# Performance work log

Hardware: AMD Instinct MI355X
Metric: run time of the kernel (lower is better)

The kernel has to match this reference:

```python
import jax, jax.numpy as jnp
import numpy as np

VOC, EDIM, HDIM, SSZ, SDIM, SDEPTH, PAD = 32000, 256, 256, 128, 128, 2, 0
N, BSZ = 64, 32
T = 2 * N - 1  # 127
N_ACTS = 2  # push, pop


def _linear(key, out_d, in_d):
    k1, k2 = jax.random.split(key)
    return (jax.random.normal(k1, (out_d, in_d), jnp.float32) * 0.02,
            jax.random.normal(k2, (out_d,), jnp.float32) * 0.02)


def setup_inputs() -> dict:
    key = jax.random.key(0)
    ks = jax.random.split(key, 9)
    emb_W = jax.random.normal(ks[0], (VOC, EDIM), jnp.float32) * 0.02
    emb_W = emb_W.at[PAD].set(0.0)  # padding_idx row is zero in torch
    W_e2h, b_e2h = _linear(ks[1], HDIM, EDIM)
    W_s2h, b_s2h = _linear(ks[2], HDIM, SDIM * SDEPTH)
    W_h2h, b_h2h = _linear(ks[3], HDIM, HDIM)
    W_h2i, b_h2i = _linear(ks[4], N_ACTS + 1, HDIM)
    W_h2s, b_h2s = _linear(ks[5], SDIM, HDIM)
    W_s2u, b_s2u = _linear(ks[6], SDIM, SDIM * SDEPTH)
    empty_elem = jax.random.normal(ks[7], (1, SDIM), jnp.float32) * 0.02
    inputs = jax.random.randint(ks[8], (N, BSZ), 0, VOC)
    return dict(inputs=inputs, emb_W=emb_W, W_e2h=W_e2h, b_e2h=b_e2h,
                W_s2h=W_s2h, b_s2h=b_s2h, W_h2h=W_h2h, b_h2h=b_h2h,
                W_h2i=W_h2i, b_h2i=b_h2i, W_h2s=W_h2s, b_h2s=b_h2s,
                W_s2u=W_s2u, b_s2u=b_s2u, empty_elem=empty_elem)


def _srnn(inputs, emb_W, W_e2h, b_e2h, W_s2h, b_s2h, W_h2h, b_h2h,
          W_h2i, b_h2i, W_h2s, b_h2s, W_s2u, b_s2u, empty_elem):
    bsz = inputs.shape[1]
    embs = emb_W[inputs]                                        # [N, bsz, edim]
    pads = jnp.broadcast_to(emb_W[PAD], (T - N, bsz, EDIM))     # padded tail
    buf0 = jnp.concatenate([embs, pads], axis=0)                # [T, bsz, edim]
    hid0 = jnp.zeros((bsz, HDIM), jnp.float32)
    stack0 = jnp.broadcast_to(empty_elem, (bsz, SSZ, SDIM))

    def step(carry, t):
        hid, stack, buf = carry
        tops = stack[:, :SDEPTH, :].reshape(bsz, SDEPTH * SDIM)
        inp = buf[t]                                            # [bsz, edim]
        ihid = inp @ W_e2h.T + b_e2h + tops @ W_s2h.T + b_s2h
        hid = jax.nn.relu(hid @ W_h2h.T + b_h2h + ihid)
        inst = ihid @ W_h2i.T + b_h2i                           # [bsz, 3]
        act = jax.nn.softmax(inst[:, :N_ACTS], axis=-1)
        gamma = 1.0 + jnp.log1p(jnp.exp(inst[:, N_ACTS:]))      # [bsz, 1]
        a = act ** gamma
        a = a / (jnp.sum(a, axis=-1, keepdims=True) + 1e-16)    # sharpened acts
        p_push, p_pop = a[:, :1], a[:, 1:]                      # [bsz, 1]
        # buffer update: pop shifts the whole buffer down one slot along time
        buf_pop = jnp.concatenate([jnp.zeros_like(buf[:1]), buf[:-1]], axis=0)
        buf = p_push[None] * buf + p_pop[None] * buf_pop        # [1,bsz,1] bcast
        push_val = jax.nn.relu(hid @ W_h2s.T + b_h2s)           # [bsz, sdim]
        u_val = jax.nn.relu(tops @ W_s2u.T + b_s2u)             # [bsz, sdim]
        z = jnp.zeros((bsz, 1, SDIM), jnp.float32)
        # W_push (shift down by 1) as an index roll
        stack_push = jnp.concatenate([z, stack[:, :-1, :]], axis=1)
        stack_push = stack_push.at[:, 0, :].add(push_val)
        # W_pop = shift up by SDEPTH, then W_push = shift down by 1
        up = jnp.concatenate([stack[:, SDEPTH:, :],
                              jnp.zeros((bsz, SDEPTH, SDIM), jnp.float32)], axis=1)
        stack_pop = jnp.concatenate([z, up[:, :-1, :]], axis=1)
        stack_pop = stack_pop.at[:, 0, :].add(u_val)
        stack_pop = stack_pop.at[:, SSZ - SDEPTH + 1:, :].add(empty_elem[0])
        stack = p_push[:, :, None] * stack_push + p_pop[:, :, None] * stack_pop
        return (hid, stack, buf), (hid, a, stack[:, 0, :])

    (hid, stack, _), (outputs, acts, top_elems) = jax.lax.scan(
        step, (hid0, stack0, buf0), jnp.arange(T))
    return outputs, hid, stack, acts, top_elems


def reference(inputs, emb_W, W_e2h, b_e2h, W_s2h, b_s2h, W_h2h, b_h2h,
              W_h2i, b_h2i, W_h2s, b_h2s, W_s2u, b_s2u, empty_elem):
    return _srnn(inputs, emb_W, W_e2h, b_e2h, W_s2h, b_s2h, W_h2h, b_h2h,
                 W_h2i, b_h2i, W_h2s, b_h2s, W_s2u, b_s2u, empty_elem)
```

## Files before the change

kernel.cpp:

```cpp
#include <hip/hip_runtime.h>
#include <stdint.h>
#include <math.h>


#define T_STEPS 127

#define OUT_OFF   0
#define HID_OFF   1040384
#define STACK_OFF 1048576
#define ACTS_OFF  1572864
#define TE_OFF    1580992

#define W3_OFF 16384
#define W2_OFF 20480
#define E2H_OFF_U 131072

typedef _Float16 h2 __attribute__((ext_vector_type(2)));

__device__ __forceinline__ unsigned packh2(float a, float b){
  h2 v; v.x = (_Float16)a; v.y = (_Float16)b;
  return __builtin_bit_cast(unsigned, v);
}
__device__ __forceinline__ float h2loF(unsigned u){ h2 v = __builtin_bit_cast(h2,u); return (float)v.x; }
__device__ __forceinline__ float h2hiF(unsigned u){ h2 v = __builtin_bit_cast(h2,u); return (float)v.y; }

#if __has_builtin(__builtin_amdgcn_fdot2)
__device__ __forceinline__ float fdot2(unsigned a, unsigned b, float c){
  return __builtin_amdgcn_fdot2(__builtin_bit_cast(h2,a), __builtin_bit_cast(h2,b), c, false);
}
#else
__device__ __forceinline__ float fdot2(unsigned a, unsigned b, float c){
  return c + h2loF(a)*h2loF(b) + h2hiF(a)*h2hiF(b);
}
#endif

#define CHOFF(u) (12*((u)>>3) + ((u)&7))
#define STGP(p)  (20*((p)>>3) + 2*((p)&7))

__global__ void prep_all(const int* __restrict__ inputs, const float* __restrict__ embW,
                         const float* __restrict__ We2h,
                         const float* __restrict__ Ws2h, const float* __restrict__ Wh2h,
                         const float* __restrict__ Wh2s, const float* __restrict__ Ws2u,
                         uint4* __restrict__ out4, unsigned* __restrict__ e2hpk){
  int tid = threadIdx.x;
  int bi  = blockIdx.x;
  if (bi >= 256){
    int gid = (bi-256)*256 + tid;
    const float* src;
    if (gid < 16384){
      int i = gid >> 10, t_ = gid & 1023;
      const float* S = (t_ < 512) ? Ws2h : Wh2h;
      int r = t_ & 511, jp = r >> 2, ks = r & 3;
      int j  = 2*jp + (i >> 3);
      int k0 = ks*64 + (i & 7)*8;
      src = S + j*256 + k0;
    } else {
      int l = gid - 16384;
      int region = l >> 12, li = l & 4095;
      int i = li >> 9, rB = li & 511;
      int jp = rB >> 3, ks = rB & 7;
      int j  = 2*jp + (i >> 2);
      int k0 = ks*32 + (i & 3)*8;
      src = (region ? Ws2u : Wh2s) + j*256 + k0;
    }
    uint4 r4;
    r4.x = packh2(src[0], src[1]); r4.y = packh2(src[2], src[3]);
    r4.z = packh2(src[4], src[5]); r4.w = packh2(src[6], src[7]);
    out4[gid] = r4;
    return;
  }
  __shared__ float emb[8][256];
  int r2 = bi >> 3, bg = bi & 7;
  for (int q=0;q<8;q++){
    int rr = q >> 2, bb = q & 3;
    int tok = inputs[(2*r2+rr)*32 + bg*4+bb];
    emb[q][tid] = embW[tok*256 + tid];
  }
  __syncthreads();
  float acc[8] = {0.f,0.f,0.f,0.f,0.f,0.f,0.f,0.f};
  for (int i8=0;i8<32;i8++){
    float4 f0 = *(const float4*)&We2h[tid*256 + i8*8];
    float4 f1 = *(const float4*)&We2h[tid*256 + i8*8 + 4];
    float wv[8] = {f0.x,f0.y,f0.z,f0.w,f1.x,f1.y,f1.z,f1.w};
    #pragma unroll
    for (int c=0;c<4;c++){
      float lo = wv[2*c], hi = wv[2*c+1];
      int k = i8*8 + c*2;
      #pragma unroll
      for (int q=0;q<8;q++)
        acc[q] += emb[q][k]*lo + emb[q][k+1]*hi;
    }
  }
  int base = (bg*4)*8192 + r2*256 + tid;
  #pragma unroll
  for (int bb=0;bb<4;bb++)
    e2hpk[base + bb*8192] = packh2(acc[bb], acc[4+bb]);
}

__global__ __attribute__((amdgpu_flat_work_group_size(1024,1024), amdgpu_waves_per_eu(4,4)))
void srnn_main(const uint4* __restrict__ ws4, const unsigned* __restrict__ wsu,
               const float* __restrict__ b_e2h, const float* __restrict__ b_s2h,
               const float* __restrict__ b_h2h, const float* __restrict__ Wh2i,
               const float* __restrict__ b_h2i, const float* __restrict__ b_h2s,
               const float* __restrict__ b_s2u, const float* __restrict__ empty_el,
               float* __restrict__ out)
{
  __shared__ __align__(16) float    stk_s[128*128];
  __shared__ __align__(16) unsigned e2h4[16*520];
  __shared__ __align__(16) float    halo_top[2][16*128];
  __shared__ __align__(16) float    halo_bot[2][16*128];
  __shared__ __align__(16) float    accih_st[320], acchp_st[320];
  __shared__ __align__(16) unsigned s_pk[192], hid_pk[192];
  __shared__ __align__(16) float    pv_s[128], uv_s[128];
  __shared__ __align__(16) float    whi_s[768];
  __shared__ float    wbuf[2][192];
  __shared__ unsigned pkwc[32];
  __shared__ float    pp_s, pq_s;

  const int tid = threadIdx.x;
  const int b   = blockIdx.x;
  const int aside = tid >> 9;
  const int ar  = tid & 511;
  const int ajp = ar >> 2;
  const int aks = ar & 3;
  const int rB  = tid & 511;
  const int jpB = rB >> 3;
  const int ksB = rB & 7;
  const int h2sSide = (tid >= 512);
  const int g   = tid >> 6;
  const int cp  = tid & 63;

  uint4 w1r[16], wBr[8];
  #pragma unroll
  for (int i=0;i<16;i++) w1r[i] = ws4[i*1024 + tid];
  {
    int wbase = h2sSide ? W3_OFF : W2_OFF;
    #pragma unroll
    for (int i=0;i<8;i++) wBr[i] = ws4[wbase + i*512 + rB];
  }

  float bA0=0.f, bA1=0.f;
  if (aks==0){
    int j0 = 2*ajp;
    if (aside==0){ bA0 = b_e2h[j0]+b_s2h[j0]; bA1 = b_e2h[j0+1]+b_s2h[j0+1]; }
    else         { bA0 = b_h2h[j0];           bA1 = b_h2h[j0+1]; }
  }
  float bB0=0.f, bB1=0.f;
  if (ksB==0){
    const float* bb = h2sSide ? b_h2s : b_s2u;
    bB0 = bb[2*jpB]; bB1 = bb[2*jpB+1];
  }
  const float bi0=b_h2i[0], bi1=b_h2i[1], bi2=b_h2i[2];

  const unsigned* e2hg = wsu + E2H_OFF_U + b*8192;
  #pragma unroll
  for (int q=0;q<8;q++){
    int idx = q*1024 + tid;
    int r2 = idx >> 8, j = idx & 255;
    e2h4[(r2>>1)*520 + 2*j + (r2&1)] = e2hg[idx];
  }
  const float2 emt2 = *(const float2*)&empty_el[2*cp];
  #pragma unroll
  for (int j=0;j<8;j++)
    *(float2*)&stk_s[(8*g+j)*128 + 2*cp] = emt2;
  *(float2*)&halo_top[0][g*128 + 2*cp] = emt2;
  *(float2*)&halo_bot[0][g*128 + 2*cp] = emt2;
  if (tid < 768) whi_s[tid] = Wh2i[tid];
  if (tid < 128){
    hid_pk[CHOFF(tid)] = 0u;
    int cu = tid & 63;
    s_pk[CHOFF(tid)] = packh2(empty_el[2*cu], empty_el[2*cu+1]);
  }
  if (tid < 192){ wbuf[0][tid] = (tid==64)?1.f:0.f; wbuf[1][tid]=0.f; }
  if (tid < 32)  pkwc[tid] = (tid==0)? packh2(1.f,0.f) : 0u;
  __syncthreads();

  int cur = 0;
  for (int t=0;t<T_STEPS;++t){
    {
      const unsigned* act  = aside ? hid_pk : s_pk;
      const unsigned* actB = act + 48*aks;
      float x0 = 0.f, x1 = 0.f;
      if (aside==0){
        #pragma unroll
        for (int qq=0;qq<4;qq++){
          int r2g = 4*aks + qq;
          unsigned cwE = pkwc[8*aks + 2*qq];
          unsigned cwO = pkwc[8*aks + 2*qq + 1];
          uint4 u = *(const uint4*)&e2h4[r2g*520 + 4*ajp];
          x0 = fdot2(cwE, u.x, x0); x0 = fdot2(cwO, u.y, x0);
          x1 = fdot2(cwE, u.z, x1); x1 = fdot2(cwO, u.w, x1);
        }
      }
      #pragma unroll
      for (int i=0;i<8;i++){
        uint4 A  = *(const uint4*)(actB + 12*(i>>1) + 4*(i&1));
        uint4 Wa = w1r[i], Wb = w1r[8+i];
        x0 = fdot2(A.x,Wa.x,x0); x0 = fdot2(A.y,Wa.y,x0);
        x0 = fdot2(A.z,Wa.z,x0); x0 = fdot2(A.w,Wa.w,x0);
        x1 = fdot2(A.x,Wb.x,x1); x1 = fdot2(A.y,Wb.y,x1);
        x1 = fdot2(A.z,Wb.z,x1); x1 = fdot2(A.w,Wb.w,x1);
      }
      x0 += __shfl_xor(x0,1); x0 += __shfl_xor(x0,2);
      x1 += __shfl_xor(x1,1); x1 += __shfl_xor(x1,2);
      if (aks==0){
        float* dst = aside ? acchp_st : accih_st;
        *(float2*)&dst[STGP(ajp)] = make_float2(x0 + bA0, x1 + bA1);
      }
    }
    __syncthreads();

    if (tid >= 64 && tid < 192){
      int hl = tid - 64;
      int w_ = STGP(hl);
      float2 ih2 = *(const float2*)&accih_st[w_];
      float2 hp2 = *(const float2*)&acchp_st[w_];
      float hn0 = fmaxf(ih2.x+hp2.x, 0.f);
      float hn1 = fmaxf(ih2.y+hp2.y, 0.f);
      hid_pk[CHOFF(hl)] = packh2(hn0,hn1);
      *(float2*)&out[OUT_OFF + t*8192 + b*256 + 2*hl] = make_float2(hn0,hn1);
      if (t==T_STEPS-1) *(float2*)&out[HID_OFF + b*256 + 2*hl] = make_float2(hn0,hn1);
    }

    {
      float y0=0.f, y1=0.f;
      #pragma unroll
      for (int i=0;i<4;i++){
        unsigned u0,u1,u2,u3;
        if (h2sSide){
          const int off = 40*ksB + ((i>=2)?20:0) + 8*(i&1);
          float4 a0 = *(const float4*)(accih_st + off);
          float4 a1 = *(const float4*)(accih_st + off + 4);
          float4 c0 = *(const float4*)(acchp_st + off);
          float4 c1 = *(const float4*)(acchp_st + off + 4);
          u0 = packh2(fmaxf(a0.x+c0.x,0.f), fmaxf(a0.y+c0.y,0.f));
          u1 = packh2(fmaxf(a0.z+c0.z,0.f), fmaxf(a0.w+c0.w,0.f));
          u2 = packh2(fmaxf(a1.x+c1.x,0.f), fmaxf(a1.y+c1.y,0.f));
          u3 = packh2(fmaxf(a1.z+c1.z,0.f), fmaxf(a1.w+c1.w,0.f));
        } else {
          uint4 S = *(const uint4*)&s_pk[12*(2*ksB + (i>>1)) + 4*(i&1)];
          u0 = S.x; u1 = S.y; u2 = S.z; u3 = S.w;
        }
        uint4 Wa = wBr[i], Wb = wBr[4+i];
        y0=fdot2(u0,Wa.x,y0); y0=fdot2(u1,Wa.y,y0); y0=fdot2(u2,Wa.z,y0); y0=fdot2(u3,Wa.w,y0);
        y1=fdot2(u0,Wb.x,y1); y1=fdot2(u1,Wb.y,y1); y1=fdot2(u2,Wb.z,y1); y1=fdot2(u3,Wb.w,y1);
      }
      y0 += __shfl_xor(y0,1); y0 += __shfl_xor(y0,2); y0 += __shfl_xor(y0,4);
      y1 += __shfl_xor(y1,1); y1 += __shfl_xor(y1,2); y1 += __shfl_xor(y1,4);
      if (ksB==0){
        float* dst = h2sSide ? pv_s : uv_s;
        dst[2*jpB]   = fmaxf(y0+bB0,0.f);
        dst[2*jpB+1] = fmaxf(y1+bB1,0.f);
      }
    }

    if (tid < 64){
      int l = tid;
      float4 av = *(const float4*)&accih_st[20*(l>>2) + 4*(l&3)];
      float4 q0 = *(const float4*)&whi_s[4*l];
      float4 q1 = *(const float4*)&whi_s[256 + 4*l];
      float4 q2 = *(const float4*)&whi_s[512 + 4*l];
      float p0 = av.x*q0.x + av.y*q0.y + av.z*q0.z + av.w*q0.w;
      float p1 = av.x*q1.x + av.y*q1.y + av.z*q1.z + av.w*q1.w;
      float p2 = av.x*q2.x + av.y*q2.y + av.z*q2.z + av.w*q2.w;
      #pragma unroll
      for (int o=1;o<=32;o<<=1){
        p0 += __shfl_xor(p0,o); p1 += __shfl_xor(p1,o); p2 += __shfl_xor(p2,o);
      }
      float i0 = bi0+p0, i1 = bi1+p1, gi = bi2+p2;
      float mx = fmaxf(i0,i1);
      float e0 = expf(i0-mx), e1 = expf(i1-mx);
      float inv = 1.f/(e0+e1);
      float act0 = e0*inv, act1 = e1*inv;
      float gamma = 1.f + log1pf(expf(gi));
      float A0 = powf(act0,gamma), A1 = powf(act1,gamma);
      float sden = A0+A1+1e-16f;
      if (l==0){
        float ppv = A0/sden, pqv = A1/sden;
        pp_s = ppv; pq_s = pqv;
        *(float2*)&out[ACTS_OFF + t*64 + b*2] = make_float2(ppv,pqv);
      }
    }
    __syncthreads();
    const float pp = pp_s, pq = pq_s;

    {
      float2 w[10];
      #pragma unroll
      for (int k=1;k<=8;k++)
        w[k] = *(const float2*)&stk_s[(8*g + k - 1)*128 + 2*cp];
      w[0] = (g>0)  ? *(const float2*)&halo_bot[cur][(g-1)*128 + 2*cp]
                    : make_float2(0.f,0.f);
      w[9] = (g<15) ? *(const float2*)&halo_top[cur][(g+1)*128 + 2*cp]
                    : emt2;
      float2 pv2 = make_float2(0.f,0.f), uv2 = make_float2(0.f,0.f);
      if (g == 0){ pv2 = *(const float2*)&pv_s[2*cp]; uv2 = *(const float2*)&uv_s[2*cp]; }
      float2 nn0, nn1;
      #pragma unroll
      for (int j=0;j<8;j++){
        float2 nv;
        nv.x = pp*w[j].x + pq*w[j+2].x;
        nv.y = pp*w[j].y + pq*w[j+2].y;
        if (j==0 && g==0){
          nv.x = pp*pv2.x + pq*uv2.x;
          nv.y = pp*pv2.y + pq*uv2.y;
        }
        *(float2*)&stk_s[(8*g+j)*128 + 2*cp] = nv;
        if (j==0){ nn0 = nv; *(float2*)&halo_top[cur^1][g*128 + 2*cp] = nv; }
        if (j==1){ nn1 = nv; }
        if (j==7){ *(float2*)&halo_bot[cur^1][g*128 + 2*cp] = nv; }
      }
      if (g == 0){
        *(float2*)&out[TE_OFF + t*4096 + b*128 + 2*cp] = nn0;
        s_pk[CHOFF(cp)]    = packh2(nn0.x, nn0.y);
        s_pk[CHOFF(64+cp)] = packh2(nn1.x, nn1.y);
      }
      if (tid < 128){
        int k = 64+tid;
        wbuf[cur^1][k] = pp*wbuf[cur][k] + pq*wbuf[cur][k-1];
      } else if (tid < 160){
        int r2 = tid-128;
        int k1 = 65 + t - 2*r2;
        float wa = wbuf[cur][k1], wb2 = wbuf[cur][k1-1], wc2 = wbuf[cur][k1-2];
        pkwc[r2] = packh2(pp*wa+pq*wb2, pp*wb2+pq*wc2);
      }
    }
    __syncthreads();
    cur ^= 1;
  }

  #pragma unroll
  for (int j=0;j<8;j++)
    *(float2*)&out[STACK_OFF + b*16384 + (8*g+j)*128 + 2*cp] =
      *(const float2*)&stk_s[(8*g+j)*128 + 2*cp];
}

extern "C" void kernel_launch(void* const* d_in, const int* in_sizes, int n_in,
                              void* d_out, int out_size, void* d_ws, size_t ws_size,
                              hipStream_t stream){
  const int*   inputs = (const int*)d_in[0];
  const float* embW   = (const float*)d_in[1];
  const float* We2h   = (const float*)d_in[2];
  const float* b_e2h  = (const float*)d_in[3];
  const float* Ws2h   = (const float*)d_in[4];
  const float* b_s2h  = (const float*)d_in[5];
  const float* Wh2h   = (const float*)d_in[6];
  const float* b_h2h  = (const float*)d_in[7];
  const float* Wh2i   = (const float*)d_in[8];
  const float* b_h2i  = (const float*)d_in[9];
  const float* Wh2s   = (const float*)d_in[10];
  const float* b_h2s  = (const float*)d_in[11];
  const float* Ws2u   = (const float*)d_in[12];
  const float* b_s2u  = (const float*)d_in[13];
  const float* empty  = (const float*)d_in[14];
  unsigned* wsu = (unsigned*)d_ws;

  prep_all<<<dim3(352), dim3(256), 0, stream>>>(inputs, embW, We2h, Ws2h, Wh2h,
                                                Wh2s, Ws2u, (uint4*)wsu,
                                                wsu + E2H_OFF_U);
  srnn_main<<<dim3(32), dim3(1024), 0, stream>>>((const uint4*)wsu, (const unsigned*)wsu,
                                                 b_e2h, b_s2h, b_h2h, Wh2i, b_h2i,
                                                 b_h2s, b_s2u, empty, (float*)d_out);
}
```

Baseline: 891.4 us.

## Precompute h2i projections to compute gates in parallel with matvec, cut a barrier

Folds W_h2i through W_s2h and the e2h projection on the host-side prep kernel so the push/pop gate can be computed from the stack top and token contributions directly, concurrently with the main matvec instead of after it. This removes one block-wide barrier per timestep and lets the h2s/s2u results feed the stack top row directly via a double-buffered row0 buffer. It adds a precompute block and extra workspace, and rearranges thread roles, with some risk of reduced precision from reassociation.

```diff
diff --git a/kernel.cpp b/kernel.cpp
--- a/kernel.cpp
+++ b/kernel.cpp
@@ -14,6 +14,9 @@
 #define W3_OFF 16384
 #define W2_OFF 20480
 #define E2H_OFF_U 131072
+#define E2I_F 393216
+#define P2_F  401408
+#define CVEC_F 402176
 
 typedef _Float16 h2 __attribute__((ext_vector_type(2)));
 
@@ -33,6 +36,8 @@
   return c + h2loF(a)*h2loF(b) + h2hiF(a)*h2hiF(b);
 }
 #endif
+
+#define BAR() asm volatile("s_waitcnt lgkmcnt(0)\n\ts_barrier" ::: "memory")
 
 #define CHOFF(u) (12*((u)>>3) + ((u)&7))
 #define STGP(p)  (20*((p)>>3) + 2*((p)&7))
@@ -41,10 +46,16 @@
                          const float* __restrict__ We2h,
                          const float* __restrict__ Ws2h, const float* __restrict__ Wh2h,
                          const float* __restrict__ Wh2s, const float* __restrict__ Ws2u,
-                         uint4* __restrict__ out4, unsigned* __restrict__ e2hpk){
+                         const float* __restrict__ Wh2i,
+                         const float* __restrict__ b_e2h, const float* __restrict__ b_s2h,
+                         const float* __restrict__ b_h2i,
+                         unsigned* __restrict__ wsu){
   int tid = threadIdx.x;
   int bi  = blockIdx.x;
-  if (bi >= 256){
+  uint4* out4 = (uint4*)wsu;
+  unsigned* e2hpk = wsu + E2H_OFF_U;
+  float* wsf = (float*)wsu;
+  if (bi >= 256 && bi < 352){
     int gid = (bi-256)*256 + tid;
     const float* src;
     if (gid < 16384){
@@ -69,7 +80,25 @@
     out4[gid] = r4;
     return;
   }
+  if (bi == 352){
+    int k = tid;
+    float s0=0.f, s1=0.f, s2=0.f;
+    for (int m=0;m<256;m++){
+      float wmk = Ws2h[m*256+k];
+      s0 += Wh2i[m]*wmk; s1 += Wh2i[256+m]*wmk; s2 += Wh2i[512+m]*wmk;
+    }
+    wsf[P2_F +       k] = s0;
+    wsf[P2_F + 256 + k] = s1;
+    wsf[P2_F + 512 + k] = s2;
+    if (tid < 3){
+      float c = b_h2i[tid];
+      for (int m=0;m<256;m++) c += (b_e2h[m]+b_s2h[m])*Wh2i[tid*256+m];
+      wsf[CVEC_F + tid] = c;
+    }
+    return;
+  }
   __shared__ float emb[8][256];
+  __shared__ float red[3][4][8];
   int r2 = bi >> 3, bg = bi & 7;
   for (int q=0;q<8;q++){
     int rr = q >> 2, bb = q & 3;
@@ -95,24 +124,48 @@
   #pragma unroll
   for (int bb=0;bb<4;bb++)
     e2hpk[base + bb*8192] = packh2(acc[bb], acc[4+bb]);
+  int wv_ = tid>>6, ln = tid&63;
+  for (int jj=0;jj<3;jj++){
+    float w = Wh2i[jj*256 + tid];
+    float v[8];
+    #pragma unroll
+    for (int q=0;q<8;q++) v[q] = acc[q]*w;
+    #pragma unroll
+    for (int o=1;o<=32;o<<=1){
+      #pragma unroll
+      for (int q=0;q<8;q++) v[q] += __shfl_xor(v[q],o);
+    }
+    if (ln==0){
+      #pragma unroll
+      for (int q=0;q<8;q++) red[jj][wv_][q] = v[q];
+    }
+  }
+  __syncthreads();
+  if (tid < 24){
+    int jj = tid>>3, q = tid&7;
+    float s = red[jj][0][q]+red[jj][1][q]+red[jj][2][q]+red[jj][3][q];
+    int rr = q>>2, bb = q&3;
+    wsf[E2I_F + (4*bg+bb)*256 + jj*64 + (2*r2+rr)] = s;
+  }
 }
 
 __global__ __attribute__((amdgpu_flat_work_group_size(1024,1024), amdgpu_waves_per_eu(4,4)))
 void srnn_main(const uint4* __restrict__ ws4, const unsigned* __restrict__ wsu,
                const float* __restrict__ b_e2h, const float* __restrict__ b_s2h,
-               const float* __restrict__ b_h2h, const float* __restrict__ Wh2i,
-               const float* __restrict__ b_h2i, const float* __restrict__ b_h2s,
-               const float* __restrict__ b_s2u, const float* __restrict__ empty_el,
-               float* __restrict__ out)
+               const float* __restrict__ b_h2h,
+               const float* __restrict__ b_h2s, const float* __restrict__ b_s2u,
+               const float* __restrict__ empty_el, float* __restrict__ out)
 {
   __shared__ __align__(16) float    stk_s[128*128];
   __shared__ __align__(16) unsigned e2h4[16*520];
   __shared__ __align__(16) float    halo_top[2][16*128];
   __shared__ __align__(16) float    halo_bot[2][16*128];
+  __shared__ __align__(16) float    row0_lds[2][128];
   __shared__ __align__(16) float    accih_st[320], acchp_st[320];
-  __shared__ __align__(16) unsigned s_pk[192], hid_pk[192];
-  __shared__ __align__(16) float    pv_s[128], uv_s[128];
-  __shared__ __align__(16) float    whi_s[768];
+  __shared__ __align__(16) unsigned s_pk[2][192];
+  __shared__ __align__(16) unsigned hid_pk[192];
+  __shared__ __align__(16) float    e2i_s[192];
+  __shared__ __align__(16) float    p2_s[768];
   __shared__ float    wbuf[2][192];
   __shared__ unsigned pkwc[32];
   __shared__ float    pp_s, pq_s;
@@ -123,10 +176,9 @@
   const int ar  = tid & 511;
   const int ajp = ar >> 2;
   const int aks = ar & 3;
-  const int rB  = tid & 511;
-  const int jpB = rB >> 3;
-  const int ksB = rB & 7;
-  const int h2sSide = (tid >= 512);
+  const int jpB = tid >> 4;
+  const int which = (tid >> 3) & 1;
+  const int ksB = tid & 7;
   const int g   = tid >> 6;
   const int cp  = tid & 63;
 
@@ -134,9 +186,10 @@
   #pragma unroll
   for (int i=0;i<16;i++) w1r[i] = ws4[i*1024 + tid];
   {
-    int wbase = h2sSide ? W3_OFF : W2_OFF;
+    int wbase = which ? W3_OFF : W2_OFF;
+    int rIdx  = jpB*8 + ksB;
     #pragma unroll
-    for (int i=0;i<8;i++) wBr[i] = ws4[wbase + i*512 + rB];
+    for (int i=0;i<8;i++) wBr[i] = ws4[wbase + i*512 + rIdx];
   }
 
   float bA0=0.f, bA1=0.f;
@@ -145,12 +198,11 @@
     if (aside==0){ bA0 = b_e2h[j0]+b_s2h[j0]; bA1 = b_e2h[j0+1]+b_s2h[j0+1]; }
     else         { bA0 = b_h2h[j0];           bA1 = b_h2h[j0+1]; }
   }
-  float bB0=0.f, bB1=0.f;
-  if (ksB==0){
-    const float* bb = h2sSide ? b_h2s : b_s2u;
-    bB0 = bb[2*jpB]; bB1 = bb[2*jpB+1];
-  }
-  const float bi0=b_h2i[0], bi1=b_h2i[1], bi2=b_h2i[2];
+  const float* bbB = which ? b_h2s : b_s2u;
+  const float bB0 = bbB[2*jpB], bB1 = bbB[2*jpB+1];
+  const float* wsf = (const float*)wsu;
+  float c0r=0.f, c1r=0.f, c2r=0.f;
+  if (tid >= 960){ c0r = wsf[CVEC_F]; c1r = wsf[CVEC_F+1]; c2r = wsf[CVEC_F+2]; }
 
   const unsigned* e2hg = wsu + E2H_OFF_U + b*8192;
   #pragma unroll
@@ -165,11 +217,13 @@
     *(float2*)&stk_s[(8*g+j)*128 + 2*cp] = emt2;
   *(float2*)&halo_top[0][g*128 + 2*cp] = emt2;
   *(float2*)&halo_bot[0][g*128 + 2*cp] = emt2;
-  if (tid < 768) whi_s[tid] = Wh2i[tid];
+  if (tid < 128) row0_lds[0][tid] = empty_el[tid];
+  if (tid < 192) e2i_s[tid] = wsf[E2I_F + b*256 + tid];
+  if (tid < 768) p2_s[tid] = wsf[P2_F + tid];
   if (tid < 128){
     hid_pk[CHOFF(tid)] = 0u;
     int cu = tid & 63;
-    s_pk[CHOFF(tid)] = packh2(empty_el[2*cu], empty_el[2*cu+1]);
+    s_pk[0][CHOFF(tid)] = packh2(empty_el[2*cu], empty_el[2*cu+1]);
   }
   if (tid < 192){ wbuf[0][tid] = (tid==64)?1.f:0.f; wbuf[1][tid]=0.f; }
   if (tid < 32)  pkwc[tid] = (tid==0)? packh2(1.f,0.f) : 0u;
@@ -178,7 +232,7 @@
   int cur = 0;
   for (int t=0;t<T_STEPS;++t){
     {
-      const unsigned* act  = aside ? hid_pk : s_pk;
+      const unsigned* act  = aside ? hid_pk : s_pk[cur];
       const unsigned* actB = act + 48*aks;
       float x0 = 0.f, x1 = 0.f;
       if (aside==0){
@@ -208,7 +262,55 @@
         *(float2*)&dst[STGP(ajp)] = make_float2(x0 + bA0, x1 + bA1);
       }
     }
-    __syncthreads();
+    if (tid >= 960){
+      int l = tid - 960;
+      float p0, p1, p2v;
+      if (l < 32){
+        unsigned cw = pkwc[l];
+        float cf0 = h2loF(cw), cf1 = h2hiF(cw);
+        float2 a0 = *(const float2*)&e2i_s[      2*l];
+        float2 a1 = *(const float2*)&e2i_s[ 64 + 2*l];
+        float2 a2 = *(const float2*)&e2i_s[128 + 2*l];
+        p0  = cf0*a0.x + cf1*a0.y;
+        p1  = cf0*a1.x + cf1*a1.y;
+        p2v = cf0*a2.x + cf1*a2.y;
+      } else {
+        int c = l - 32;
+        p0 = p1 = p2v = 0.f;
+        #pragma unroll
+        for (int m=0;m<4;m++){
+          int k2 = c + 32*m;
+          unsigned tp = s_pk[cur][CHOFF(k2)];
+          float t0 = h2loF(tp), t1 = h2hiF(tp);
+          float2 q0 = *(const float2*)&p2_s[      2*k2];
+          float2 q1 = *(const float2*)&p2_s[256 + 2*k2];
+          float2 q2 = *(const float2*)&p2_s[512 + 2*k2];
+          p0  += t0*q0.x + t1*q0.y;
+          p1  += t0*q1.x + t1*q1.y;
+          p2v += t0*q2.x + t1*q2.y;
+        }
+      }
+      #pragma unroll
+      for (int o=1;o<=32;o<<=1){
+        p0 += __shfl_xor(p0,o); p1 += __shfl_xor(p1,o); p2v += __shfl_xor(p2v,o);
+      }
+      if (l == 0){
+        float i0 = c0r+p0, i1 = c1r+p1, gi = c2r+p2v;
+        float mx = fmaxf(i0,i1);
+        float e0 = expf(i0-mx), e1 = expf(i1-mx);
+        float inv = 1.f/(e0+e1);
+        float act0 = e0*inv, act1 = e1*inv;
+        float gamma = 1.f + log1pf(expf(gi));
+        float A0 = powf(act0,gamma), A1 = powf(act1,gamma);
+        float sden = A0+A1+1e-16f;
+        float ppv = A0/sden, pqv = A1/sden;
+        pp_s = ppv; pq_s = pqv;
+        *(float2*)&out[ACTS_OFF + t*64 + b*2] = make_float2(ppv,pqv);
+      }
+    }
+    BAR();
+
+    const float pp = pp_s, pq = pq_s;
 
     if (tid >= 64 && tid < 192){
       int hl = tid - 64;
@@ -227,7 +329,7 @@
       #pragma unroll
       for (int i=0;i<4;i++){
         unsigned u0,u1,u2,u3;
-        if (h2sSide){
+        if (which){
           const int off = 40*ksB + ((i>=2)?20:0) + 8*(i&1);
           float4 a0 = *(const float4*)(accih_st + off);
           float4 a1 = *(const float4*)(accih_st + off + 4);
@@ -238,7 +340,7 @@
           u2 = packh2(fmaxf(a1.x+c1.x,0.f), fmaxf(a1.y+c1.y,0.f));
           u3 = packh2(fmaxf(a1.z+c1.z,0.f), fmaxf(a1.w+c1.w,0.f));
         } else {
-          uint4 S = *(const uint4*)&s_pk[12*(2*ksB + (i>>1)) + 4*(i&1)];
+          uint4 S = *(const uint4*)&s_pk[cur][12*(2*ksB + (i>>1)) + 4*(i&1)];
           u0 = S.x; u1 = S.y; u2 = S.z; u3 = S.w;
         }
         uint4 Wa = wBr[i], Wb = wBr[4+i];
@@ -247,92 +349,61 @@
       }
       y0 += __shfl_xor(y0,1); y0 += __shfl_xor(y0,2); y0 += __shfl_xor(y0,4);
       y1 += __shfl_xor(y1,1); y1 += __shfl_xor(y1,2); y1 += __shfl_xor(y1,4);
-      if (ksB==0){
-        float* dst = h2sSide ? pv_s : uv_s;
-        dst[2*jpB]   = fmaxf(y0+bB0,0.f);
-        dst[2*jpB+1] = fmaxf(y1+bB1,0.f);
-      }
-    }
-
-    if (tid < 64){
-      int l = tid;
-      float4 av = *(const float4*)&accih_st[20*(l>>2) + 4*(l&3)];
-      float4 q0 = *(const float4*)&whi_s[4*l];
-      float4 q1 = *(const float4*)&whi_s[256 + 4*l];
-      float4 q2 = *(const float4*)&whi_s[512 + 4*l];
-      float p0 = av.x*q0.x + av.y*q0.y + av.z*q0.z + av.w*q0.w;
-      float p1 = av.x*q1.x + av.y*q1.y + av.z*q1.z + av.w*q1.w;
-      float p2 = av.x*q2.x + av.y*q2.y + av.z*q2.z + av.w*q2.w;
-      #pragma unroll
-      for (int o=1;o<=32;o<<=1){
-        p0 += __shfl_xor(p0,o); p1 += __shfl_xor(p1,o); p2 += __shfl_xor(p2,o);
-      }
-      float i0 = bi0+p0, i1 = bi1+p1, gi = bi2+p2;
-      float mx = fmaxf(i0,i1);
-      float e0 = expf(i0-mx), e1 = expf(i1-mx);
-      float inv = 1.f/(e0+e1);
-      float act0 = e0*inv, act1 = e1*inv;
-      float gamma = 1.f + log1pf(expf(gi));
-      float A0 = powf(act0,gamma), A1 = powf(act1,gamma);
-      float sden = A0+A1+1e-16f;
-      if (l==0){
-        float ppv = A0/sden, pqv = A1/sden;
-        pp_s = ppv; pq_s = pqv;
-        *(float2*)&out[ACTS_OFF + t*64 + b*2] = make_float2(ppv,pqv);
-      }
-    }
-    __syncthreads();
-    const float pp = pp_s, pq = pq_s;
+      float v0 = fmaxf(y0+bB0, 0.f), v1 = fmaxf(y1+bB1, 0.f);
+      float o0 = __shfl_xor(v0, 8),  o1 = __shfl_xor(v1, 8);
+      if (!which && ksB==0){
+        float n0 = pp*o0 + pq*v0;
+        float n1 = pp*o1 + pq*v1;
+        *(float2*)&row0_lds[cur^1][2*jpB] = make_float2(n0,n1);
+        s_pk[cur^1][CHOFF(jpB)] = packh2(n0,n1);
+        *(float2*)&out[TE_OFF + t*4096 + b*128 + 2*jpB] = make_float2(n0,n1);
+      }
+    }
+
+    if (tid < 128){
+      int k = 64+tid;
+      wbuf[cur^1][k] = pp*wbuf[cur][k] + pq*wbuf[cur][k-1];
+    } else if (tid < 160){
+      int r2 = tid-128;
+      int k1 = 65 + t - 2*r2;
+      float wa = wbuf[cur][k1], wb2 = wbuf[cur][k1-1], wc2 = wbuf[cur][k1-2];
+      pkwc[r2] = packh2(pp*wa+pq*wb2, pp*wb2+pq*wc2);
+    }
 
     {
       float2 w[10];
       #pragma unroll
       for (int k=1;k<=8;k++)
         w[k] = *(const float2*)&stk_s[(8*g + k - 1)*128 + 2*cp];
+      if (g==0) w[1] = *(const float2*)&row0_lds[cur][2*cp];
       w[0] = (g>0)  ? *(const float2*)&halo_bot[cur][(g-1)*128 + 2*cp]
                     : make_float2(0.f,0.f);
       w[9] = (g<15) ? *(const float2*)&halo_top[cur][(g+1)*128 + 2*cp]
                     : emt2;
-      float2 pv2 = make_float2(0.f,0.f), uv2 = make_float2(0.f,0.f);
-      if (g == 0){ pv2 = *(const float2*)&pv_s[2*cp]; uv2 = *(const float2*)&uv_s[2*cp]; }
-      float2 nn0, nn1;
       #pragma unroll
       for (int j=0;j<8;j++){
+        if (j==0 && g==0) continue;
         float2 nv;
         nv.x = pp*w[j].x + pq*w[j+2].x;
         nv.y = pp*w[j].y + pq*w[j+2].y;
-        if (j==0 && g==0){
-          nv.x = pp*pv2.x + pq*uv2.x;
-          nv.y = pp*pv2.y + pq*uv2.y;
-        }
         *(float2*)&stk_s[(8*g+j)*128 + 2*cp] = nv;
-        if (j==0){ nn0 = nv; *(float2*)&halo_top[cur^1][g*128 + 2*cp] = nv; }
-        if (j==1){ nn1 = nv; }
-        if (j==7){ *(float2*)&halo_bot[cur^1][g*128 + 2*cp] = nv; }
-      }
-      if (g == 0){
-        *(float2*)&out[TE_OFF + t*4096 + b*128 + 2*cp] = nn0;
-        s_pk[CHOFF(cp)]    = packh2(nn0.x, nn0.y);
-        s_pk[CHOFF(64+cp)] = packh2(nn1.x, nn1.y);
-      }
-      if (tid < 128){
-        int k = 64+tid;
-        wbuf[cur^1][k] = pp*wbuf[cur][k] + pq*wbuf[cur][k-1];
-      } else if (tid < 160){
-        int r2 = tid-128;
-        int k1 = 65 + t - 2*r2;
-        float wa = wbuf[cur][k1], wb2 = wbuf[cur][k1-1], wc2 = wbuf[cur][k1-2];
-        pkwc[r2] = packh2(pp*wa+pq*wb2, pp*wb2+pq*wc2);
-      }
-    }
-    __syncthreads();
+        if (j==0) *(float2*)&halo_top[cur^1][g*128 + 2*cp] = nv;
+        if (j==7) *(float2*)&halo_bot[cur^1][g*128 + 2*cp] = nv;
+        if (j==1 && g==0) s_pk[cur^1][CHOFF(64+cp)] = packh2(nv.x, nv.y);
+      }
+    }
+    BAR();
     cur ^= 1;
   }
 
   #pragma unroll
-  for (int j=0;j<8;j++)
-    *(float2*)&out[STACK_OFF + b*16384 + (8*g+j)*128 + 2*cp] =
-      *(const float2*)&stk_s[(8*g+j)*128 + 2*cp];
+  for (int j=0;j<8;j++){
+    int r = 8*g + j;
+    float2 v;
+    if (g==0 && j==0) v = *(const float2*)&row0_lds[cur][2*cp];
+    else              v = *(const float2*)&stk_s[r*128 + 2*cp];
+    *(float2*)&out[STACK_OFF + b*16384 + r*128 + 2*cp] = v;
+  }
 }
 
 extern "C" void kernel_launch(void* const* d_in, const int* in_sizes, int n_in,
@@ -355,10 +426,10 @@
   const float* empty  = (const float*)d_in[14];
   unsigned* wsu = (unsigned*)d_ws;
 
-  prep_all<<<dim3(352), dim3(256), 0, stream>>>(inputs, embW, We2h, Ws2h, Wh2h,
-                                                Wh2s, Ws2u, (uint4*)wsu,
-                                                wsu + E2H_OFF_U);
+  prep_all<<<dim3(353), dim3(256), 0, stream>>>(inputs, embW, We2h, Ws2h, Wh2h,
+                                                Wh2s, Ws2u, Wh2i, b_e2h, b_s2h,
+                                                b_h2i, wsu);
   srnn_main<<<dim3(32), dim3(1024), 0, stream>>>((const uint4*)wsu, (const unsigned*)wsu,
-                                                 b_e2h, b_s2h, b_h2h, Wh2i, b_h2i,
+                                                 b_e2h, b_s2h, b_h2h,
                                                  b_h2s, b_s2u, empty, (float*)d_out);
 }
```

After: 1.014 ms. 13.7% more time.
